# Performance work log

Hardware: AMD Instinct MI355X
Metric: run time of the kernel (lower is better)

Reference implementation:

```python
import jax, jax.numpy as jnp
import numpy as np

IN_CH = 256
INTER_CH = IN_CH // 2  # reduction=2


def setup_inputs() -> dict:
    key = jax.random.key(0)
    ks = jax.random.split(key, 9)
    x = jax.random.normal(ks[0], (8, IN_CH, 64, 64), dtype=jnp.float32)
    std = 0.01
    # 1x1 conv weights stored as [out_ch, in_ch] (kernel is 1x1)
    Wg = jax.random.normal(ks[1], (INTER_CH, IN_CH), dtype=jnp.float32) * std
    bg = jnp.zeros((INTER_CH,), dtype=jnp.float32)
    Wt = jax.random.normal(ks[2], (INTER_CH, IN_CH), dtype=jnp.float32) * std
    bt = jnp.zeros((INTER_CH,), dtype=jnp.float32)
    Wp = jax.random.normal(ks[3], (INTER_CH, IN_CH), dtype=jnp.float32) * std
    bp = jnp.zeros((INTER_CH,), dtype=jnp.float32)
    # conv_out is zero-initialized in the module; use small random values so
    Wo = jax.random.normal(ks[4], (IN_CH, INTER_CH), dtype=jnp.float32) * std
    bo = jnp.zeros((IN_CH,), dtype=jnp.float32)
    return {"x": x, "Wg": Wg, "bg": bg, "Wt": Wt, "bt": bt,
            "Wp": Wp, "bp": bp, "Wo": Wo, "bo": bo}


def reference(x, Wg, bg, Wt, bt, Wp, bp, Wo, bo):
    n, c, h, w = x.shape
    s = h * w
    xf = x.reshape(n, c, s)  # [n, C, S]
    # 1x1 conv projections (no downsample, embedded_gaussian mode)
    g_x = jnp.einsum('kc,ncs->nsk', Wg, xf) + bg          # [n, S, K]
    theta_x = jnp.einsum('kc,ncs->nsk', Wt, xf) + bt      # [n, S, K]
    phi_x = jnp.einsum('kc,ncs->nks', Wp, xf) + bp[:, None]  # [n, K, S]
    # embedded_gaussian: scores -> scale (fixbug: / sqrt(K)) -> /temp(=1) -> softmax
    scale = 1.0 / jnp.sqrt(jnp.asarray(INTER_CH, dtype=x.dtype))
    scores = jnp.einsum('nsk,nkt->nst', theta_x, phi_x) * scale  # [n, S, S]
    pw = jax.nn.softmax(scores, axis=-1)
    y = jnp.einsum('nst,ntk->nsk', pw, g_x)               # [n, S, K]
    out = xf + jnp.einsum('ck,nsk->ncs', Wo, y) + bo[None, :, None]
    return out.reshape(n, c, h, w)
```

## Files before the change

kernel.cpp:

```cpp
#include <hip/hip_runtime.h>
#include <hip/hip_bf16.h>

#define NB   8
#define CCH  256
#define KCH  128
#define SSP  4096

typedef unsigned short u16;
typedef __attribute__((ext_vector_type(8))) short  bfrag;
typedef __attribute__((ext_vector_type(4))) float  ffrag;

#define MFMA16(a, b, c) __builtin_amdgcn_mfma_f32_16x16x32_bf16((a), (b), (c), 0, 0, 0)
#define SWZ(i, r) ((unsigned)(i) ^ ((((unsigned)(r)) & 7u) << 3))

#define GLDS(G, L) __builtin_amdgcn_global_load_lds(                          \
    (const __attribute__((address_space(1))) void*)(G),                       \
    (__attribute__((address_space(3))) void*)(L), 16, 0, 0)

__device__ __forceinline__ u16 f2b(float f) {
    union { float f; unsigned u; } v; v.f = f;
    return (u16)((v.u + 0x7fffu + ((v.u >> 16) & 1u)) >> 16);
}

__global__ __launch_bounds__(256, 2) void proj_gp_kernel(
    const float* __restrict__ x,
    const float* __restrict__ Wg, const float* __restrict__ bg,
    const float* __restrict__ Wp, const float* __restrict__ bp,
    u16* __restrict__ G,
    u16* __restrict__ P)
{
    __shared__ __align__(16) u16 sm[12800];
    const int tid  = threadIdx.x;
    const int wv   = tid >> 6;
    const int lane = tid & 63;
    const int quad = lane >> 4, l16 = lane & 15;
    const int bid  = blockIdx.x;
    const int n  = bid & 7;
    const int s0 = (bid >> 3) * 64;

    const ffrag zf = {0.f, 0.f, 0.f, 0.f};
    ffrag ga[8], pa[8];
#pragma unroll
    for (int kb = 0; kb < 8; kb++) { ga[kb] = zf; pa[kb] = zf; }

    float4 xreg[2], wgreg[4], wpreg[4];
#pragma unroll
    for (int i = 0; i < 2; i++) {
        int f = tid + i * 256;
        int c = f >> 4, s4 = (f & 15) * 4;
        xreg[i] = *(const float4*)&x[((size_t)n * CCH + c) * SSP + s0 + s4];
    }
#pragma unroll
    for (int i = 0; i < 4; i++) {
        int f = tid + i * 256;
        int k = f >> 3, co = (f & 7) * 4;
        wgreg[i] = *(const float4*)&Wg[k * CCH + co];
        wpreg[i] = *(const float4*)&Wp[k * CCH + co];
    }

    for (int c0 = 0; c0 < CCH; c0 += 32) {
        __syncthreads();
#pragma unroll
        for (int i = 0; i < 2; i++) {
            int f = tid + i * 256;
            int c = f >> 4, s4 = (f & 15) * 4;
            sm[(s4 + 0) * 40 + c] = f2b(xreg[i].x);
            sm[(s4 + 1) * 40 + c] = f2b(xreg[i].y);
            sm[(s4 + 2) * 40 + c] = f2b(xreg[i].z);
            sm[(s4 + 3) * 40 + c] = f2b(xreg[i].w);
        }
#pragma unroll
        for (int i = 0; i < 4; i++) {
            int f = tid + i * 256;
            int k = f >> 3, co = (f & 7) * 4;
            ushort4 g4 = {f2b(wgreg[i].x), f2b(wgreg[i].y), f2b(wgreg[i].z), f2b(wgreg[i].w)};
            ushort4 p4 = {f2b(wpreg[i].x), f2b(wpreg[i].y), f2b(wpreg[i].z), f2b(wpreg[i].w)};
            *(ushort4*)&sm[2560 + k * 40 + co] = g4;
            *(ushort4*)&sm[7680 + k * 40 + co] = p4;
        }
        if (c0 + 32 < CCH) {
#pragma unroll
            for (int i = 0; i < 2; i++) {
                int f = tid + i * 256;
                int c = f >> 4, s4 = (f & 15) * 4;
                xreg[i] = *(const float4*)&x[((size_t)n * CCH + c0 + 32 + c) * SSP + s0 + s4];
            }
#pragma unroll
            for (int i = 0; i < 4; i++) {
                int f = tid + i * 256;
                int k = f >> 3, co = (f & 7) * 4;
                wgreg[i] = *(const float4*)&Wg[k * CCH + c0 + 32 + co];
                wpreg[i] = *(const float4*)&Wp[k * CCH + c0 + 32 + co];
            }
        }
        __syncthreads();
        bfrag a = *(const bfrag*)&sm[(16 * wv + l16) * 40 + quad * 8];
#pragma unroll
        for (int kb = 0; kb < 8; kb++) {
            bfrag bgf = *(const bfrag*)&sm[2560 + (16 * kb + l16) * 40 + quad * 8];
            bfrag bpf = *(const bfrag*)&sm[7680 + (16 * kb + l16) * 40 + quad * 8];
            ga[kb] = MFMA16(a, bgf, ga[kb]);
            pa[kb] = MFMA16(a, bpf, pa[kb]);
        }
    }
#pragma unroll
    for (int kb = 0; kb < 8; kb++) {
        int k = l16 + 16 * kb;
        float bgv = bg[k], bpv = bp[k];
        int srow = s0 + 16 * wv + quad * 4;
        ushort4 g4 = {f2b(ga[kb][0] + bgv), f2b(ga[kb][1] + bgv),
                      f2b(ga[kb][2] + bgv), f2b(ga[kb][3] + bgv)};
        *(ushort4*)&G[(size_t)n * KCH * SSP + (size_t)k * SSP + srow] = g4;
#pragma unroll
        for (int r = 0; r < 4; r++)
            P[((size_t)n * SSP + srow + r) * KCH + k] = f2b(pa[kb][r] + bpv);
    }
}

__global__ __launch_bounds__(256, 2) void attn_fused_kernel(
    const float* __restrict__ x,
    const float* __restrict__ Wt, const float* __restrict__ bt,
    const u16* __restrict__ Pb,
    const u16* __restrict__ Gt,
    const float* __restrict__ Wo, const float* __restrict__ bo,
    float* __restrict__ out)
{
    __shared__ __align__(16) u16 sm[36864];
    const int tid  = threadIdx.x;
    const int wv   = tid >> 6;
    const int lane = tid & 63;
    const int quad = lane >> 4, l16 = lane & 15;
    const int bid  = blockIdx.x;
    const int n    = bid & 7;
    const int q0   = (bid >> 3) * 64;
    const float qscale = 0.08838834764831845f * 1.4426950408889634f;
    const ffrag zf = {0.f, 0.f, 0.f, 0.f};

    const int KS0b = 0, KS1b = 8192, GT0b = 16384, GT1b = 24576, PSb = 32768;
    const int XTb = 8192, WTb = 10752, QSb = 8192, WOb = 24576;

    const u16* Pbase = Pb + (size_t)n * SSP * KCH;
    const u16* Gbase = Gt + (size_t)n * KCH * SSP;

#define STAGE_TILE(KSw, GTw, T0)                                             \
    {                                                                        \
        _Pragma("unroll")                                                    \
        for (int i = 0; i < 4; i++) {                                        \
            int chunk = wv * 4 + i;                                          \
            int row = chunk * 4 + (lane >> 4);                               \
            int cs  = ((lane & 15) * 8) ^ ((row & 7) << 3);                  \
            GLDS(Pbase + (size_t)((T0) + row) * KCH + cs,                    \
                 &sm[(KSw) + chunk * 512]);                                  \
        }                                                                    \
        _Pragma("unroll")                                                    \
        for (int i = 0; i < 4; i++) {                                        \
            int chunk = wv * 4 + i;                                          \
            int k  = chunk * 8 + (lane >> 3);                                \
            int cs = ((lane & 7) * 8) ^ ((k & 7) << 3);                      \
            GLDS(Gbase + (size_t)k * SSP + (T0) + cs,                        \
                 &sm[(GTw) + chunk * 512]);                                  \
        }                                                                    \
    }

    STAGE_TILE(KS0b, GT0b, 0)

    {
        ffrag qa[8];
#pragma unroll
        for (int kb = 0; kb < 8; kb++) qa[kb] = zf;

        for (int c0 = 0; c0 < CCH; c0 += 32) {
#pragma unroll
            for (int i = 0; i < 2; i++) {
                int f = tid + i * 256;
                int c = f >> 4, s4 = (f & 15) * 4;
                float4 xv = *(const float4*)&x[((size_t)n * CCH + c0 + c) * SSP + q0 + s4];
                sm[XTb + (s4 + 0) * 40 + c] = f2b(xv.x);
                sm[XTb + (s4 + 1) * 40 + c] = f2b(xv.y);
                sm[XTb + (s4 + 2) * 40 + c] = f2b(xv.z);
                sm[XTb + (s4 + 3) * 40 + c] = f2b(xv.w);
            }
#pragma unroll
            for (int i = 0; i < 4; i++) {
                int f = tid + i * 256;
                int k = f >> 3, co = (f & 7) * 4;
                float4 wq4 = *(const float4*)&Wt[k * CCH + c0 + co];
                ushort4 q4 = {f2b(wq4.x), f2b(wq4.y), f2b(wq4.z), f2b(wq4.w)};
                *(ushort4*)&sm[WTb + k * 40 + co] = q4;
            }
            __syncthreads();
            bfrag aq = *(const bfrag*)&sm[XTb + (16 * wv + l16) * 40 + quad * 8];
#pragma unroll
            for (int kb = 0; kb < 8; kb++) {
                bfrag bw = *(const bfrag*)&sm[WTb + (16 * kb + l16) * 40 + quad * 8];
                qa[kb] = MFMA16(aq, bw, qa[kb]);
            }
            __syncthreads();
        }
#pragma unroll
        for (int kb = 0; kb < 8; kb++) {
            float btv = bt[l16 + 16 * kb];
#pragma unroll
            for (int r = 0; r < 4; r++) {
                int row = 16 * wv + quad * 4 + r;
                sm[QSb + SWZ(row * 128 + l16 + 16 * kb, row)] = f2b((qa[kb][r] + btv) * qscale);
            }
        }
    }

    bfrag qf[4];
#pragma unroll
    for (int kc = 0; kc < 4; kc++)
        qf[kc] = *(const bfrag*)&sm[QSb + SWZ((16 * wv + l16) * 128 + kc * 32 + quad * 8, l16)];

    asm volatile("s_waitcnt vmcnt(0) lgkmcnt(0)" ::: "memory");
    __builtin_amdgcn_s_barrier();

    ffrag O[8];
#pragma unroll
    for (int kb = 0; kb < 8; kb++) O[kb] = zf;
    float l_r[4] = {0.f, 0.f, 0.f, 0.f};

    const int NT = SSP / 64;
#pragma unroll 2
    for (int it = 0; it < NT; ++it) {
        const int cur = it & 1;
        const int KS  = cur ? KS1b : KS0b;
        const int GT  = cur ? GT1b : GT0b;

        if (it + 1 < NT) {
            const int KSw = cur ? KS0b : KS1b;
            const int GTw = cur ? GT0b : GT1b;
            STAGE_TILE(KSw, GTw, (it + 1) * 64)
        }

        ffrag sa[4];
#pragma unroll
        for (int tb = 0; tb < 4; tb++) sa[tb] = zf;
#pragma unroll
        for (int kc = 0; kc < 4; kc++)
#pragma unroll
            for (int tb = 0; tb < 4; tb++) {
                bfrag bk = *(const bfrag*)&sm[KS + SWZ((16 * tb + l16) * 128 + kc * 32 + quad * 8, l16)];
                sa[tb] = MFMA16(qf[kc], bk, sa[tb]);
            }

#pragma unroll
        for (int r = 0; r < 4; r++) {
            float p0 = __builtin_amdgcn_exp2f(sa[0][r]);
            float p1 = __builtin_amdgcn_exp2f(sa[1][r]);
            float p2 = __builtin_amdgcn_exp2f(sa[2][r]);
            float p3 = __builtin_amdgcn_exp2f(sa[3][r]);
            l_r[r] += (p0 + p1) + (p2 + p3);
            int row = 16 * wv + quad * 4 + r;
            int rb = row * 64 + l16;
            sm[PSb + SWZ(rb +  0, row)] = f2b(p0);
            sm[PSb + SWZ(rb + 16, row)] = f2b(p1);
            sm[PSb + SWZ(rb + 32, row)] = f2b(p2);
            sm[PSb + SWZ(rb + 48, row)] = f2b(p3);
        }

#pragma unroll
        for (int tc = 0; tc < 2; tc++) {
            bfrag ap = *(const bfrag*)&sm[PSb + SWZ((16 * wv + l16) * 64 + tc * 32 + quad * 8, l16)];
#pragma unroll
            for (int kb = 0; kb < 8; kb++) {
                bfrag bg = *(const bfrag*)&sm[GT + SWZ((16 * kb + l16) * 64 + tc * 32 + quad * 8, l16)];
                O[kb] = MFMA16(ap, bg, O[kb]);
            }
        }

        asm volatile("s_waitcnt vmcnt(0) lgkmcnt(0)" ::: "memory");
        __builtin_amdgcn_s_barrier();
    }
#undef STAGE_TILE

    {
        float rs0 = l_r[0], rs1 = l_r[1], rs2 = l_r[2], rs3 = l_r[3];
#pragma unroll
        for (int m = 1; m <= 8; m <<= 1) {
            rs0 += __shfl_xor(rs0, m);
            rs1 += __shfl_xor(rs1, m);
            rs2 += __shfl_xor(rs2, m);
            rs3 += __shfl_xor(rs3, m);
        }
        float lr0 = 1.0f / rs0, lr1 = 1.0f / rs1, lr2 = 1.0f / rs2, lr3 = 1.0f / rs3;
#pragma unroll
        for (int kb = 0; kb < 8; kb++) {
            int rowb = 16 * wv + quad * 4;
            sm[QSb + SWZ((rowb + 0) * 128 + l16 + 16 * kb, rowb + 0)] = f2b(O[kb][0] * lr0);
            sm[QSb + SWZ((rowb + 1) * 128 + l16 + 16 * kb, rowb + 1)] = f2b(O[kb][1] * lr1);
            sm[QSb + SWZ((rowb + 2) * 128 + l16 + 16 * kb, rowb + 2)] = f2b(O[kb][2] * lr2);
            sm[QSb + SWZ((rowb + 3) * 128 + l16 + 16 * kb, rowb + 3)] = f2b(O[kb][3] * lr3);
        }
    }

#pragma unroll
    for (int qtr = 0; qtr < 4; qtr++) {
        __syncthreads();
#pragma unroll
        for (int i = 0; i < 8; i++) {
            int f = tid + i * 256;
            int c = f >> 5, ko = (f & 31) * 4;
            float4 w = *(const float4*)&Wo[(size_t)(qtr * 64 + c) * KCH + ko];
            ushort4 w4 = {f2b(w.x), f2b(w.y), f2b(w.z), f2b(w.w)};
            *(ushort4*)&sm[WOb + SWZ(c * 128 + ko, c)] = w4;
        }
        __syncthreads();

        ffrag zc[4];
#pragma unroll
        for (int cb = 0; cb < 4; cb++) zc[cb] = zf;
#pragma unroll
        for (int kc = 0; kc < 4; kc++) {
            bfrag ay = *(const bfrag*)&sm[QSb + SWZ((16 * wv + l16) * 128 + kc * 32 + quad * 8, l16)];
#pragma unroll
            for (int cb = 0; cb < 4; cb++) {
                bfrag bw = *(const bfrag*)&sm[WOb + SWZ((16 * cb + l16) * 128 + kc * 32 + quad * 8, l16)];
                zc[cb] = MFMA16(ay, bw, zc[cb]);
            }
        }
#pragma unroll
        for (int cb = 0; cb < 4; cb++) {
            int c = qtr * 64 + 16 * cb + l16;
            float bc = bo[c];
            size_t base = ((size_t)n * CCH + c) * SSP + q0 + 16 * wv + quad * 4;
            float4 xv = *(const float4*)&x[base];
            float4 ov;
            ov.x = xv.x + zc[cb][0] + bc;
            ov.y = xv.y + zc[cb][1] + bc;
            ov.z = xv.z + zc[cb][2] + bc;
            ov.w = xv.w + zc[cb][3] + bc;
            *(float4*)&out[base] = ov;
        }
    }
}

extern "C" void kernel_launch(void* const* d_in, const int* in_sizes, int n_in,
                              void* d_out, int out_size, void* d_ws, size_t ws_size,
                              hipStream_t stream) {
    const float* x  = (const float*)d_in[0];
    const float* Wg = (const float*)d_in[1];
    const float* bg = (const float*)d_in[2];
    const float* Wt = (const float*)d_in[3];
    const float* bt = (const float*)d_in[4];
    const float* Wp = (const float*)d_in[5];
    const float* bp = (const float*)d_in[6];
    const float* Wo = (const float*)d_in[7];
    const float* bo = (const float*)d_in[8];
    float* out = (float*)d_out;

    u16* G = (u16*)d_ws;
    u16* P = G + (size_t)NB * SSP * KCH;

    proj_gp_kernel<<<dim3(NB * SSP / 64), 256, 0, stream>>>(x, Wg, bg, Wp, bp, G, P);
    attn_fused_kernel<<<dim3(NB * SSP / 64), 256, 0, stream>>>(x, Wt, bt, P, G, Wo, bo, out);
}
```

Before: 217.6 us.

## Split attention key tiles across wave pairs and double-buffer projection LDS

The projection kernel now keeps two LDS buffers, so the commit of the next channel chunk overlaps the MFMA work on the current one, with one barrier per iteration instead of two. The attention kernel changes its wave layout: each wave handles 32 query rows and half of every 64-key tile, so each K and G fragment read from LDS feeds two MFMAs. This cuts LDS read traffic per MFMA. In exchange, each wave carries twice as many output accumulators, which adds register pressure, and the two partial outputs and row sums must be merged through LDS in fp32 with an extra barrier before the output projection.

```diff
diff --git a/kernel.cpp b/kernel.cpp
--- a/kernel.cpp
+++ b/kernel.cpp
@@ -29,7 +29,7 @@
     u16* __restrict__ G,
     u16* __restrict__ P)
 {
-    __shared__ __align__(16) u16 sm[12800];
+    __shared__ __align__(16) u16 sm[25600];
     const int tid  = threadIdx.x;
     const int wv   = tid >> 6;
     const int lane = tid & 63;
@@ -44,65 +44,72 @@
     for (int kb = 0; kb < 8; kb++) { ga[kb] = zf; pa[kb] = zf; }
 
     float4 xreg[2], wgreg[4], wpreg[4];
-#pragma unroll
-    for (int i = 0; i < 2; i++) {
-        int f = tid + i * 256;
-        int c = f >> 4, s4 = (f & 15) * 4;
-        xreg[i] = *(const float4*)&x[((size_t)n * CCH + c) * SSP + s0 + s4];
-    }
-#pragma unroll
-    for (int i = 0; i < 4; i++) {
-        int f = tid + i * 256;
-        int k = f >> 3, co = (f & 7) * 4;
-        wgreg[i] = *(const float4*)&Wg[k * CCH + co];
-        wpreg[i] = *(const float4*)&Wp[k * CCH + co];
-    }
-
-    for (int c0 = 0; c0 < CCH; c0 += 32) {
-        __syncthreads();
-#pragma unroll
-        for (int i = 0; i < 2; i++) {
-            int f = tid + i * 256;
-            int c = f >> 4, s4 = (f & 15) * 4;
-            sm[(s4 + 0) * 40 + c] = f2b(xreg[i].x);
-            sm[(s4 + 1) * 40 + c] = f2b(xreg[i].y);
-            sm[(s4 + 2) * 40 + c] = f2b(xreg[i].z);
-            sm[(s4 + 3) * 40 + c] = f2b(xreg[i].w);
-        }
-#pragma unroll
-        for (int i = 0; i < 4; i++) {
-            int f = tid + i * 256;
-            int k = f >> 3, co = (f & 7) * 4;
-            ushort4 g4 = {f2b(wgreg[i].x), f2b(wgreg[i].y), f2b(wgreg[i].z), f2b(wgreg[i].w)};
-            ushort4 p4 = {f2b(wpreg[i].x), f2b(wpreg[i].y), f2b(wpreg[i].z), f2b(wpreg[i].w)};
-            *(ushort4*)&sm[2560 + k * 40 + co] = g4;
-            *(ushort4*)&sm[7680 + k * 40 + co] = p4;
-        }
-        if (c0 + 32 < CCH) {
-#pragma unroll
-            for (int i = 0; i < 2; i++) {
-                int f = tid + i * 256;
-                int c = f >> 4, s4 = (f & 15) * 4;
-                xreg[i] = *(const float4*)&x[((size_t)n * CCH + c0 + 32 + c) * SSP + s0 + s4];
-            }
-#pragma unroll
-            for (int i = 0; i < 4; i++) {
-                int f = tid + i * 256;
-                int k = f >> 3, co = (f & 7) * 4;
-                wgreg[i] = *(const float4*)&Wg[k * CCH + c0 + 32 + co];
-                wpreg[i] = *(const float4*)&Wp[k * CCH + c0 + 32 + co];
-            }
-        }
-        __syncthreads();
-        bfrag a = *(const bfrag*)&sm[(16 * wv + l16) * 40 + quad * 8];
+
+#define K1_LOAD(C0)                                                          \
+    {                                                                        \
+        _Pragma("unroll")                                                    \
+        for (int i = 0; i < 2; i++) {                                        \
+            int f = tid + i * 256;                                           \
+            int c = f >> 4, s4 = (f & 15) * 4;                               \
+            xreg[i] = *(const float4*)&x[((size_t)n * CCH + (C0) + c) * SSP + s0 + s4]; \
+        }                                                                    \
+        _Pragma("unroll")                                                    \
+        for (int i = 0; i < 4; i++) {                                        \
+            int f = tid + i * 256;                                           \
+            int k = f >> 3, co = (f & 7) * 4;                                \
+            wgreg[i] = *(const float4*)&Wg[k * CCH + (C0) + co];             \
+            wpreg[i] = *(const float4*)&Wp[k * CCH + (C0) + co];             \
+        }                                                                    \
+    }
+
+#define K1_COMMIT(B)                                                         \
+    {                                                                        \
+        const int bb = (B) * 12800;                                          \
+        _Pragma("unroll")                                                    \
+        for (int i = 0; i < 2; i++) {                                        \
+            int f = tid + i * 256;                                           \
+            int c = f >> 4, s4 = (f & 15) * 4;                               \
+            sm[bb + (s4 + 0) * 40 + c] = f2b(xreg[i].x);                     \
+            sm[bb + (s4 + 1) * 40 + c] = f2b(xreg[i].y);                     \
+            sm[bb + (s4 + 2) * 40 + c] = f2b(xreg[i].z);                     \
+            sm[bb + (s4 + 3) * 40 + c] = f2b(xreg[i].w);                     \
+        }                                                                    \
+        _Pragma("unroll")                                                    \
+        for (int i = 0; i < 4; i++) {                                        \
+            int f = tid + i * 256;                                           \
+            int k = f >> 3, co = (f & 7) * 4;                                \
+            ushort4 g4 = {f2b(wgreg[i].x), f2b(wgreg[i].y), f2b(wgreg[i].z), f2b(wgreg[i].w)}; \
+            ushort4 p4 = {f2b(wpreg[i].x), f2b(wpreg[i].y), f2b(wpreg[i].z), f2b(wpreg[i].w)}; \
+            *(ushort4*)&sm[bb + 2560 + k * 40 + co] = g4;                    \
+            *(ushort4*)&sm[bb + 7680 + k * 40 + co] = p4;                    \
+        }                                                                    \
+    }
+
+    K1_LOAD(0)
+    K1_COMMIT(0)
+    K1_LOAD(32)
+    asm volatile("s_waitcnt lgkmcnt(0)" ::: "memory");
+    __builtin_amdgcn_s_barrier();
+
+#pragma unroll
+    for (int it = 0; it < 8; ++it) {
+        if (it < 7) K1_COMMIT((it + 1) & 1)
+        if (it < 6) K1_LOAD((it + 2) * 32)
+        const int bb = (it & 1) * 12800;
+        bfrag a = *(const bfrag*)&sm[bb + (16 * wv + l16) * 40 + quad * 8];
 #pragma unroll
         for (int kb = 0; kb < 8; kb++) {
-            bfrag bgf = *(const bfrag*)&sm[2560 + (16 * kb + l16) * 40 + quad * 8];
-            bfrag bpf = *(const bfrag*)&sm[7680 + (16 * kb + l16) * 40 + quad * 8];
+            bfrag bgf = *(const bfrag*)&sm[bb + 2560 + (16 * kb + l16) * 40 + quad * 8];
+            bfrag bpf = *(const bfrag*)&sm[bb + 7680 + (16 * kb + l16) * 40 + quad * 8];
             ga[kb] = MFMA16(a, bgf, ga[kb]);
             pa[kb] = MFMA16(a, bpf, pa[kb]);
         }
-    }
+        asm volatile("s_waitcnt lgkmcnt(0)" ::: "memory");
+        __builtin_amdgcn_s_barrier();
+    }
+#undef K1_LOAD
+#undef K1_COMMIT
+
 #pragma unroll
     for (int kb = 0; kb < 8; kb++) {
         int k = l16 + 16 * kb;
@@ -130,6 +137,8 @@
     const int wv   = tid >> 6;
     const int lane = tid & 63;
     const int quad = lane >> 4, l16 = lane & 15;
+    const int wq   = wv & 1;
+    const int tpar = wv >> 1;
     const int bid  = blockIdx.x;
     const int n    = bid & 7;
     const int q0   = (bid >> 3) * 64;
@@ -137,7 +146,8 @@
     const ffrag zf = {0.f, 0.f, 0.f, 0.f};
 
     const int KS0b = 0, KS1b = 8192, GT0b = 16384, GT1b = 24576, PSb = 32768;
-    const int XTb = 8192, WTb = 10752, QSb = 8192, WOb = 24576;
+    const int XTb = 8192, WTb = 10752, QSb = 8192;
+    const int YSb = 24576, WOb = 16384;
 
     const u16* Pbase = Pb + (size_t)n * SSP * KCH;
     const u16* Gbase = Gt + (size_t)n * KCH * SSP;
@@ -207,19 +217,28 @@
             }
         }
     }
-
-    bfrag qf[4];
-#pragma unroll
-    for (int kc = 0; kc < 4; kc++)
-        qf[kc] = *(const bfrag*)&sm[QSb + SWZ((16 * wv + l16) * 128 + kc * 32 + quad * 8, l16)];
+    __syncthreads();
+
+    bfrag qf[2][4];
+#pragma unroll
+    for (int qb = 0; qb < 2; qb++)
+#pragma unroll
+        for (int kc = 0; kc < 4; kc++)
+            qf[qb][kc] = *(const bfrag*)&sm[QSb + SWZ((32 * wq + 16 * qb + l16) * 128 + kc * 32 + quad * 8, l16)];
 
     asm volatile("s_waitcnt vmcnt(0) lgkmcnt(0)" ::: "memory");
     __builtin_amdgcn_s_barrier();
 
-    ffrag O[8];
-#pragma unroll
-    for (int kb = 0; kb < 8; kb++) O[kb] = zf;
-    float l_r[4] = {0.f, 0.f, 0.f, 0.f};
+    ffrag O[2][8];
+#pragma unroll
+    for (int qb = 0; qb < 2; qb++)
+#pragma unroll
+        for (int kb = 0; kb < 8; kb++) O[qb][kb] = zf;
+    float l_r[2][4];
+#pragma unroll
+    for (int qb = 0; qb < 2; qb++)
+#pragma unroll
+        for (int r = 0; r < 4; r++) l_r[qb][r] = 0.f;
 
     const int NT = SSP / 64;
 #pragma unroll 2
@@ -234,39 +253,41 @@
             STAGE_TILE(KSw, GTw, (it + 1) * 64)
         }
 
-        ffrag sa[4];
-#pragma unroll
-        for (int tb = 0; tb < 4; tb++) sa[tb] = zf;
+        ffrag sa[2][2];
+#pragma unroll
+        for (int qb = 0; qb < 2; qb++)
+#pragma unroll
+            for (int tb = 0; tb < 2; tb++) sa[qb][tb] = zf;
 #pragma unroll
         for (int kc = 0; kc < 4; kc++)
 #pragma unroll
-            for (int tb = 0; tb < 4; tb++) {
-                bfrag bk = *(const bfrag*)&sm[KS + SWZ((16 * tb + l16) * 128 + kc * 32 + quad * 8, l16)];
-                sa[tb] = MFMA16(qf[kc], bk, sa[tb]);
-            }
-
-#pragma unroll
-        for (int r = 0; r < 4; r++) {
-            float p0 = __builtin_amdgcn_exp2f(sa[0][r]);
-            float p1 = __builtin_amdgcn_exp2f(sa[1][r]);
-            float p2 = __builtin_amdgcn_exp2f(sa[2][r]);
-            float p3 = __builtin_amdgcn_exp2f(sa[3][r]);
-            l_r[r] += (p0 + p1) + (p2 + p3);
-            int row = 16 * wv + quad * 4 + r;
-            int rb = row * 64 + l16;
-            sm[PSb + SWZ(rb +  0, row)] = f2b(p0);
-            sm[PSb + SWZ(rb + 16, row)] = f2b(p1);
-            sm[PSb + SWZ(rb + 32, row)] = f2b(p2);
-            sm[PSb + SWZ(rb + 48, row)] = f2b(p3);
-        }
-
-#pragma unroll
-        for (int tc = 0; tc < 2; tc++) {
-            bfrag ap = *(const bfrag*)&sm[PSb + SWZ((16 * wv + l16) * 64 + tc * 32 + quad * 8, l16)];
+            for (int tb = 0; tb < 2; tb++) {
+                bfrag bk = *(const bfrag*)&sm[KS + SWZ((16 * (2 * tpar + tb) + l16) * 128 + kc * 32 + quad * 8, l16)];
+                sa[0][tb] = MFMA16(qf[0][kc], bk, sa[0][tb]);
+                sa[1][tb] = MFMA16(qf[1][kc], bk, sa[1][tb]);
+            }
+
+#pragma unroll
+        for (int qb = 0; qb < 2; qb++)
+#pragma unroll
+            for (int r = 0; r < 4; r++) {
+                float p0 = __builtin_amdgcn_exp2f(sa[qb][0][r]);
+                float p1 = __builtin_amdgcn_exp2f(sa[qb][1][r]);
+                l_r[qb][r] += p0 + p1;
+                int row = 32 * wq + 16 * qb + quad * 4 + r;
+                int cb0 = row * 64 + l16 + 32 * tpar;
+                sm[PSb + SWZ(cb0,      row)] = f2b(p0);
+                sm[PSb + SWZ(cb0 + 16, row)] = f2b(p1);
+            }
+
+        {
+            bfrag ap0 = *(const bfrag*)&sm[PSb + SWZ((32 * wq + l16) * 64 + 32 * tpar + quad * 8, l16)];
+            bfrag ap1 = *(const bfrag*)&sm[PSb + SWZ((32 * wq + 16 + l16) * 64 + 32 * tpar + quad * 8, l16)];
 #pragma unroll
             for (int kb = 0; kb < 8; kb++) {
-                bfrag bg = *(const bfrag*)&sm[GT + SWZ((16 * kb + l16) * 64 + tc * 32 + quad * 8, l16)];
-                O[kb] = MFMA16(ap, bg, O[kb]);
+                bfrag bg = *(const bfrag*)&sm[GT + SWZ((16 * kb + l16) * 64 + 32 * tpar + quad * 8, l16)];
+                O[0][kb] = MFMA16(ap0, bg, O[0][kb]);
+                O[1][kb] = MFMA16(ap1, bg, O[1][kb]);
             }
         }
 
@@ -275,24 +296,49 @@
     }
 #undef STAGE_TILE
 
-    {
-        float rs0 = l_r[0], rs1 = l_r[1], rs2 = l_r[2], rs3 = l_r[3];
-#pragma unroll
-        for (int m = 1; m <= 8; m <<= 1) {
-            rs0 += __shfl_xor(rs0, m);
-            rs1 += __shfl_xor(rs1, m);
-            rs2 += __shfl_xor(rs2, m);
-            rs3 += __shfl_xor(rs3, m);
-        }
-        float lr0 = 1.0f / rs0, lr1 = 1.0f / rs1, lr2 = 1.0f / rs2, lr3 = 1.0f / rs3;
-#pragma unroll
-        for (int kb = 0; kb < 8; kb++) {
-            int rowb = 16 * wv + quad * 4;
-            sm[QSb + SWZ((rowb + 0) * 128 + l16 + 16 * kb, rowb + 0)] = f2b(O[kb][0] * lr0);
-            sm[QSb + SWZ((rowb + 1) * 128 + l16 + 16 * kb, rowb + 1)] = f2b(O[kb][1] * lr1);
-            sm[QSb + SWZ((rowb + 2) * 128 + l16 + 16 * kb, rowb + 2)] = f2b(O[kb][2] * lr2);
-            sm[QSb + SWZ((rowb + 3) * 128 + l16 + 16 * kb, rowb + 3)] = f2b(O[kb][3] * lr3);
-        }
+#pragma unroll
+    for (int qb = 0; qb < 2; qb++)
+#pragma unroll
+        for (int r = 0; r < 4; r++) {
+            float rs = l_r[qb][r];
+#pragma unroll
+            for (int m = 1; m <= 8; m <<= 1) rs += __shfl_xor(rs, m);
+            l_r[qb][r] = rs;
+        }
+    float* smf = (float*)sm;
+    if (tpar == 1) {
+#pragma unroll
+        for (int qb = 0; qb < 2; qb++)
+#pragma unroll
+            for (int kb = 0; kb < 8; kb++)
+#pragma unroll
+                for (int r = 0; r < 4; r++) {
+                    int row = 32 * wq + 16 * qb + quad * 4 + r;
+                    smf[row * 128 + 16 * kb + l16] = O[qb][kb][r];
+                }
+        if (l16 == 0) {
+#pragma unroll
+            for (int qb = 0; qb < 2; qb++)
+#pragma unroll
+                for (int r = 0; r < 4; r++)
+                    smf[16384 + 32 * wq + 16 * qb + quad * 4 + r] = l_r[qb][r];
+        }
+    }
+    __syncthreads();
+    if (tpar == 0) {
+#pragma unroll
+        for (int qb = 0; qb < 2; qb++)
+#pragma unroll
+            for (int r = 0; r < 4; r++) {
+                int row = 32 * wq + 16 * qb + quad * 4 + r;
+                float linv = 1.0f / (l_r[qb][r] + smf[16384 + row]);
+#pragma unroll
+                for (int kb = 0; kb < 8; kb++) {
+                    int col = 16 * kb + l16;
+                    float o = O[qb][kb][r] + smf[row * 128 + col];
+                    sm[YSb + SWZ(row * 128 + col, row)] = f2b(o * linv);
+                }
+            }
     }
 
 #pragma unroll
@@ -313,7 +359,7 @@
         for (int cb = 0; cb < 4; cb++) zc[cb] = zf;
 #pragma unroll
         for (int kc = 0; kc < 4; kc++) {
-            bfrag ay = *(const bfrag*)&sm[QSb + SWZ((16 * wv + l16) * 128 + kc * 32 + quad * 8, l16)];
+            bfrag ay = *(const bfrag*)&sm[YSb + SWZ((16 * wv + l16) * 128 + kc * 32 + quad * 8, l16)];
 #pragma unroll
             for (int cb = 0; cb < 4; cb++) {
                 bfrag bw = *(const bfrag*)&sm[WOb + SWZ((16 * cb + l16) * 128 + kc * 32 + quad * 8, l16)];
```

New measurement: 216.5 us. About the same (-0.5%).
